# Optimization experiments

Hardware: AMD Instinct MI355X
Metric: run time of the kernel (lower is better)

Reference implementation:

```python
import jax, jax.numpy as jnp
import numpy as np
import math

B, NX, NY = 2, 2048, 2048
CX, CY = 1024, 1024
KEY_CH, VAL_CH, HEADS = 1024, 1024, 16


def setup_inputs() -> dict:
    key = jax.random.key(0)
    ks = jax.random.split(key, 10)
    s = lambda fan_in: 1.0 / math.sqrt(fan_in)
    inp = {
        "x": jax.random.normal(ks[0], (B, NX, CX), dtype=jnp.float32),
        "y": jax.random.normal(ks[1], (B, NY, CY), dtype=jnp.float32),
        "Wq": jax.random.uniform(ks[2], (CX, KEY_CH), jnp.float32, -s(CX), s(CX)),
        "bq": jax.random.uniform(ks[3], (KEY_CH,), jnp.float32, -s(CX), s(CX)),
        "Wk": jax.random.uniform(ks[4], (CY, KEY_CH), jnp.float32, -s(CY), s(CY)),
        "bk": jax.random.uniform(ks[5], (KEY_CH,), jnp.float32, -s(CY), s(CY)),
        "Wv": jax.random.uniform(ks[6], (CY, VAL_CH), jnp.float32, -s(CY), s(CY)),
        "bv": jax.random.uniform(ks[7], (VAL_CH,), jnp.float32, -s(CY), s(CY)),
        "Wo": jax.random.uniform(ks[8], (VAL_CH, CX), jnp.float32, -s(VAL_CH), s(VAL_CH)),
        "bo": jax.random.uniform(ks[9], (CX,), jnp.float32, -s(VAL_CH), s(VAL_CH)),
    }
    return inp


def reference(x, y, Wq, bq, Wk, bk, Wv, bv, Wo, bo):
    Bx, Nx, _ = x.shape
    By, Ny, _ = y.shape
    dk = KEY_CH // HEADS
    dv = VAL_CH // HEADS
    # projections
    q = (x @ Wq + bq).reshape(Bx, Nx, HEADS, dk)  # contiguous head slices == reshape
    k = (y @ Wk + bk).reshape(By, Ny, HEADS, dk)
    v = (y @ Wv + bv).reshape(By, Ny, HEADS, dv)
    # NOTE: original scales by 1/sqrt(Ny) (sequence length), not 1/sqrt(dk)
    scores = jnp.einsum("bnhd,bmhd->bhnm", q, k) / jnp.sqrt(jnp.float32(Ny))
    attn = jax.nn.softmax(scores, axis=-1)
    out = jnp.einsum("bhnm,bmhd->bnhd", attn, v).reshape(Bx, Nx, VAL_CH)
    out = jax.nn.relu(out @ Wo + bo)
    # dropout(p=0.2) is identity in eval mode
    return out
```

## Files before the change

kernel.cpp:

```cpp
#include <hip/hip_runtime.h>
#include <hip/hip_bf16.h>

typedef __bf16 bf16;
typedef __attribute__((ext_vector_type(8))) __bf16 bf16x8;
typedef __attribute__((ext_vector_type(4))) __bf16 bf16x4;
typedef __attribute__((ext_vector_type(4))) float f32x4;
typedef __attribute__((ext_vector_type(16))) float f32x16;
typedef __attribute__((ext_vector_type(4))) unsigned int u32x4;

__device__ __forceinline__ void gload_lds16(const void* g, void* l) {
  __builtin_amdgcn_global_load_lds((const __attribute__((address_space(1))) void*)g,
                                   (__attribute__((address_space(3))) void*)l, 16, 0, 0);
}

__device__ __forceinline__ float exp2_fast(float x) {
  float r;
  asm("v_exp_f32 %0, %1" : "=v"(r) : "v"(x));
  return r;
}

__device__ __forceinline__ unsigned cvtpk(float lo, float hi) {
  unsigned r;
  asm("v_cvt_pk_bf16_f32 %0, %1, %2" : "=v"(r) : "v"(lo), "v"(hi));
  return r;
}

__device__ __forceinline__ void plswap(unsigned& a, unsigned& b) {
  asm("v_permlane32_swap_b32 %0, %1" : "+v"(a), "+v"(b));
}

__global__ __launch_bounds__(256) void cvtw_kernel(
    const float* __restrict__ x, const float* __restrict__ y,
    bf16* __restrict__ xb, bf16* __restrict__ yb,
    const float* __restrict__ W0, const float* __restrict__ W1,
    const float* __restrict__ W2, const float* __restrict__ W3,
    bf16* __restrict__ T0, bf16* __restrict__ T1,
    bf16* __restrict__ T2, bf16* __restrict__ T3) {
  __shared__ float t[32][33];
  const int bid = blockIdx.x, tid = threadIdx.x;
  if (bid < 4096) {
    const int z = bid >> 10, rem = bid & 1023;
    const int bx = rem & 31, by = rem >> 5;
    const float* W; bf16* T;
    switch (z) {
      case 0: W = W0; T = T0; break;
      case 1: W = W1; T = T1; break;
      case 2: W = W2; T = T2; break;
      default: W = W3; T = T3; break;
    }
    const int tx = tid & 31, ty = tid >> 5;
    const int bn = bx * 32, bk = by * 32;
#pragma unroll
    for (int i = 0; i < 32; i += 8)
      t[ty + i][tx] = W[(size_t)(bk + ty + i) * 1024 + bn + tx];
    __syncthreads();
#pragma unroll
    for (int i = 0; i < 32; i += 8)
      T[(size_t)(bn + ty + i) * 1024 + bk + tx] = (bf16)t[tx][ty + i];
  } else {
    const int n4 = 1048576;
    int i = (bid - 4096) * 256 + tid;
    const float4* in = (const float4*)x; bf16x4* out = (bf16x4*)xb;
    if (i >= n4) { in = (const float4*)y; out = (bf16x4*)yb; i -= n4; }
    float4 v = in[i];
    bf16x4 o;
    o[0] = (bf16)v.x; o[1] = (bf16)v.y; o[2] = (bf16)v.z; o[3] = (bf16)v.w;
    out[i] = o;
  }
}

__global__ __launch_bounds__(512, 6) void gemm_qkv(
    const bf16* __restrict__ xb, const bf16* __restrict__ yb,
    const bf16* __restrict__ Wqt, const bf16* __restrict__ Wkt, const bf16* __restrict__ Wvt,
    const float* __restrict__ bq, const float* __restrict__ bk, const float* __restrict__ bv,
    bf16* __restrict__ Qb, bf16* __restrict__ Kb, bf16* __restrict__ Vtb) {
  constexpr int K = 1024;
  constexpr float QSCALE = (float)(1.4426950408889634 / 45.254833995939045);
  __shared__ bf16 As[2][128 * 32];
  __shared__ bf16 Bs[2][128 * 32];
  const int z = blockIdx.z;
  const bf16* A  = (z == 0) ? xb : yb;
  const bf16* Bt = (z == 0) ? Wqt : (z == 1) ? Wkt : Wvt;
  const float* bias = (z == 0) ? bq : (z == 1) ? bk : bv;

  const int tid = threadIdx.x;
  const int wave = tid >> 6, lane = tid & 63;
  const int g = lane >> 4, r15 = lane & 15;
  const int m0 = blockIdx.x * 128, n0 = blockIdx.y * 128;
  const int wr = wave >> 2, wc = wave & 3;

  f32x4 acc[4][2] = {};

  const int rowA = tid >> 2, chA = tid & 3;

  auto stage = [&](int buf, int k0) {
    gload_lds16(A  + (size_t)(m0 + rowA) * K + k0 + chA * 8, (char*)As[buf] + tid * 16);
    gload_lds16(Bt + (size_t)(n0 + rowA) * K + k0 + chA * 8, (char*)Bs[buf] + tid * 16);
  };

  stage(0, 0);
  __syncthreads();
  int cur = 0;
  for (int t = 0; t < K / 32; ++t) {
    if (t + 1 < K / 32) stage(cur ^ 1, (t + 1) * 32);
    bf16x8 af[4], bfr[2];
#pragma unroll
    for (int mi = 0; mi < 4; ++mi)
      af[mi] = *(const bf16x8*)((const char*)As[cur] + ((wr * 64 + mi * 16 + r15) * 64 + g * 16));
#pragma unroll
    for (int nj = 0; nj < 2; ++nj)
      bfr[nj] = *(const bf16x8*)((const char*)Bs[cur] + ((wc * 32 + nj * 16 + r15) * 64 + g * 16));
#pragma unroll
    for (int mi = 0; mi < 4; ++mi)
#pragma unroll
      for (int nj = 0; nj < 2; ++nj)
        acc[mi][nj] = __builtin_amdgcn_mfma_f32_16x16x32_bf16(af[mi], bfr[nj], acc[mi][nj], 0, 0, 0);
    __syncthreads();
    cur ^= 1;
  }

  const float scl = (z == 0) ? QSCALE : 1.0f;
#pragma unroll
  for (int mi = 0; mi < 4; ++mi) {
#pragma unroll
    for (int nj = 0; nj < 2; ++nj) {
      int row = m0 + wr * 64 + mi * 16 + g * 4;
      int col = n0 + wc * 32 + nj * 16 + r15;
      float bv_ = bias[col];
      if (z < 2) {
        bf16* C = (z == 0) ? Qb : Kb;
#pragma unroll
        for (int r = 0; r < 4; ++r)
          C[(size_t)(row + r) * 1024 + col] = (bf16)((acc[mi][nj][r] + bv_) * scl);
      } else {
        int b = row >> 11, n = row & 2047;
        bf16x4 pkv;
#pragma unroll
        for (int r = 0; r < 4; ++r)
          pkv[r] = (bf16)(acc[mi][nj][r] + bv_);
        *(bf16x4*)(Vtb + ((size_t)b * 1024 + col) * 2048 + n) = pkv;
      }
    }
  }
}

__global__ __launch_bounds__(512, 4) void gemm_out(
    const bf16* __restrict__ A, const bf16* __restrict__ Bt,
    const float* __restrict__ bias, float* __restrict__ C) {
  constexpr int K = 1024;
  __shared__ bf16 As[2][128 * 32];
  __shared__ bf16 Bs[2][64 * 32];
  const int tid = threadIdx.x;
  const int wave = tid >> 6, lane = tid & 63;
  const int g = lane >> 4, r15 = lane & 15;
  const int m0 = blockIdx.x * 128, n0 = blockIdx.y * 64;
  const int wr = wave >> 1, wc = wave & 1;

  f32x4 acc[2][2] = {};

  const int rowA = tid >> 2, chA = tid & 3;

  auto stage = [&](int buf, int k0) {
    gload_lds16(A + (size_t)(m0 + rowA) * K + k0 + chA * 8, (char*)As[buf] + tid * 16);
    if (tid < 256)
      gload_lds16(Bt + (size_t)(n0 + rowA) * K + k0 + chA * 8, (char*)Bs[buf] + tid * 16);
  };

  stage(0, 0);
  __syncthreads();
  int cur = 0;
  for (int t = 0; t < K / 32; ++t) {
    if (t + 1 < K / 32) stage(cur ^ 1, (t + 1) * 32);
    bf16x8 af[2], bfr[2];
#pragma unroll
    for (int mi = 0; mi < 2; ++mi)
      af[mi] = *(const bf16x8*)((const char*)As[cur] + ((wr * 32 + mi * 16 + r15) * 64 + g * 16));
#pragma unroll
    for (int nj = 0; nj < 2; ++nj)
      bfr[nj] = *(const bf16x8*)((const char*)Bs[cur] + ((wc * 32 + nj * 16 + r15) * 64 + g * 16));
#pragma unroll
    for (int mi = 0; mi < 2; ++mi)
#pragma unroll
      for (int nj = 0; nj < 2; ++nj)
        acc[mi][nj] = __builtin_amdgcn_mfma_f32_16x16x32_bf16(af[mi], bfr[nj], acc[mi][nj], 0, 0, 0);
    __syncthreads();
    cur ^= 1;
  }

#pragma unroll
  for (int mi = 0; mi < 2; ++mi)
#pragma unroll
    for (int nj = 0; nj < 2; ++nj) {
      int row = m0 + wr * 32 + mi * 16 + g * 4;
      int col = n0 + wc * 32 + nj * 16 + r15;
      float bv_ = bias[col];
#pragma unroll
      for (int r = 0; r < 4; ++r)
        C[(size_t)(row + r) * 1024 + col] = fmaxf(acc[mi][nj][r] + bv_, 0.0f);
    }
}

__global__ __launch_bounds__(128, 2) void attn_kernel(
    const bf16* __restrict__ Q, const bf16* __restrict__ Kin,
    const bf16* __restrict__ Vt, bf16* __restrict__ Oa) {
  __shared__ bf16 Ks[2][64 * 64];
  __shared__ bf16 Vs[2][64 * 64];
  __shared__ float lsh[2][2][32];
  const int tid = threadIdx.x;
  const int w = tid >> 6, lane = tid & 63;
  const int q5 = lane & 31, h = lane >> 5;

  int i = blockIdx.y * 32 + blockIdx.x;
  int xcd = i & 7, slot = i >> 3;
  int bh = xcd * 4 + (slot >> 5), qt = slot & 31;
  int b = bh >> 4, hd = bh & 15;

  const bf16* Qg = Q + ((size_t)b * 2048 + qt * 64) * 1024 + hd * 64;
  const bf16* Kg = Kin + (size_t)b * 2048 * 1024 + hd * 64;
  const bf16* Vg = Vt + ((size_t)b * 1024 + hd * 64) * 2048;

  bf16x8 qf[2][4];
#pragma unroll
  for (int qb = 0; qb < 2; ++qb)
#pragma unroll
    for (int ks = 0; ks < 4; ++ks)
      qf[qb][ks] = *(const bf16x8*)(Qg + (size_t)(qb * 32 + q5) * 1024 + ks * 16 + h * 8);

  f32x16 o[2][2] = {};
  float ls[2] = {};

  auto stage = [&](int buf, int kv0) {
#pragma unroll
    for (int ii = 0; ii < 4; ++ii) {
      int c = tid + ii * 128;
      int row = c >> 3;
      int sl = (c & 7) ^ (row & 7) ^ ((row >> 3) & 1);
      gload_lds16(Kg + (size_t)(kv0 + row) * 1024 + sl * 8, (char*)Ks[buf] + c * 16);
      gload_lds16(Vg + (size_t)row * 2048 + kv0 + sl * 8, (char*)Vs[buf] + c * 16);
    }
  };

  stage(0, 0);
  __syncthreads();
  int cur = 0;

  const int krow = w * 32 + q5;
  const int kswz = (krow & 7) ^ ((krow >> 3) & 1);

  unsigned uA[2][8], uB[2][8];
  bf16x8 vA[4], vB[4];

  auto phase = [&](int t, unsigned (&uin)[2][8], unsigned (&uout)[2][8],
                   bf16x8 (&vin)[4], bf16x8 (&vout)[4], bool doStage, bool doPV) {
    if (doStage) stage(cur ^ 1, (t + 1) * 64);

    f32x16 s[2] = {};
    __builtin_amdgcn_s_setprio(1);
#pragma unroll
    for (int ks = 0; ks < 4; ++ks) {
      bf16x8 kf = *(const bf16x8*)((const char*)Ks[cur] + krow * 128 + (((2 * ks + h) ^ kswz) << 4));
      s[0] = __builtin_amdgcn_mfma_f32_32x32x16_bf16(kf, qf[0][ks], s[0], 0, 0, 0);
      s[1] = __builtin_amdgcn_mfma_f32_32x32x16_bf16(kf, qf[1][ks], s[1], 0, 0, 0);
    }

#pragma unroll
    for (int j = 0; j < 2; ++j) {
      const int db = w ^ j;
      const int vrow0 = db * 32 + q5;
      const int vswz = (vrow0 & 7) ^ ((vrow0 >> 3) & 1);
#pragma unroll
      for (int kap = 0; kap < 2; ++kap)
        vout[2 * j + kap] = *(const bf16x8*)((const char*)Vs[cur] + vrow0 * 128 +
                                             (((4 * w + 2 * kap + h) ^ vswz) << 4));
    }

    if (doPV) {
#pragma unroll
      for (int j = 0; j < 2; ++j)
#pragma unroll
        for (int kap = 0; kap < 2; ++kap)
#pragma unroll
          for (int qb = 0; qb < 2; ++qb) {
            u32x4 uw;
            uw[0] = uin[qb][4 * kap + 0]; uw[1] = uin[qb][4 * kap + 1];
            uw[2] = uin[qb][4 * kap + 2]; uw[3] = uin[qb][4 * kap + 3];
            bf16x8 pa = __builtin_bit_cast(bf16x8, uw);
            o[qb][j] = __builtin_amdgcn_mfma_f32_32x32x16_bf16(pa, vin[2 * j + kap], o[qb][j], 0, 0, 0);
          }
    }
    __builtin_amdgcn_s_setprio(0);

#pragma unroll
    for (int qb = 0; qb < 2; ++qb) {
      float e[16];
#pragma unroll
      for (int jj = 0; jj < 16; ++jj) e[jj] = exp2_fast(s[qb][jj]);
      ls[qb] += ((((e[0] + e[1]) + (e[2] + e[3])) + ((e[4] + e[5]) + (e[6] + e[7]))) +
                 (((e[8] + e[9]) + (e[10] + e[11])) + ((e[12] + e[13]) + (e[14] + e[15]))));
#pragma unroll
      for (int p = 0; p < 8; ++p) uout[qb][p] = cvtpk(e[2 * p], e[2 * p + 1]);
      plswap(uout[qb][0], uout[qb][2]); plswap(uout[qb][1], uout[qb][3]);
      plswap(uout[qb][4], uout[qb][6]); plswap(uout[qb][5], uout[qb][7]);
    }

    __syncthreads();
    cur ^= 1;
  };

  phase(0, uB, uA, vB, vA, true, false);
  for (int t = 1; t < 31; t += 2) {
    phase(t, uA, uB, vA, vB, true, true);
    phase(t + 1, uB, uA, vB, vA, true, true);
  }
  phase(31, uA, uB, vA, vB, false, true);
#pragma unroll
  for (int j = 0; j < 2; ++j)
#pragma unroll
    for (int kap = 0; kap < 2; ++kap)
#pragma unroll
      for (int qb = 0; qb < 2; ++qb) {
        u32x4 uw;
        uw[0] = uB[qb][4 * kap + 0]; uw[1] = uB[qb][4 * kap + 1];
        uw[2] = uB[qb][4 * kap + 2]; uw[3] = uB[qb][4 * kap + 3];
        bf16x8 pa = __builtin_bit_cast(bf16x8, uw);
        o[qb][j] = __builtin_amdgcn_mfma_f32_32x32x16_bf16(pa, vB[2 * j + kap], o[qb][j], 0, 0, 0);
      }

  ls[0] += __shfl_xor(ls[0], 32);
  ls[1] += __shfl_xor(ls[1], 32);
  if (h == 0) { lsh[w][0][q5] = ls[0]; lsh[w][1][q5] = ls[1]; }

  float* osh = (float*)Ks;
#pragma unroll
  for (int qb = 0; qb < 2; ++qb)
    *(f32x16*)(osh + ((w * 2 + qb) * 64 + lane) * 16) = o[qb][1];
  __syncthreads();

#pragma unroll
  for (int qb = 0; qb < 2; ++qb) {
    float lt = ls[qb] + lsh[1 - w][qb][q5];
    float iv = __builtin_amdgcn_rcpf(lt);
    f32x16 p = *(const f32x16*)(osh + (((1 - w) * 2 + qb) * 64 + lane) * 16);
#pragma unroll
    for (int g4 = 0; g4 < 4; ++g4)
#pragma unroll
      for (int r = 0; r < 4; ++r) {
        int qr = g4 * 8 + 4 * h + r;
        float il = __shfl(iv, qr);
        size_t row = (size_t)b * 2048 + qt * 64 + qb * 32 + qr;
        Oa[row * 1024 + hd * 64 + w * 32 + q5] = (bf16)((o[qb][0][g4 * 4 + r] + p[g4 * 4 + r]) * il);
      }
  }
}

extern "C" void kernel_launch(void* const* d_in, const int* in_sizes, int n_in,
                              void* d_out, int out_size, void* d_ws, size_t ws_size,
                              hipStream_t stream) {
  (void)in_sizes; (void)n_in; (void)out_size; (void)ws_size;
  const float* x  = (const float*)d_in[0];
  const float* y  = (const float*)d_in[1];
  const float* Wq = (const float*)d_in[2];
  const float* bq = (const float*)d_in[3];
  const float* Wk = (const float*)d_in[4];
  const float* bk = (const float*)d_in[5];
  const float* Wv = (const float*)d_in[6];
  const float* bv = (const float*)d_in[7];
  const float* Wo = (const float*)d_in[8];
  const float* bo = (const float*)d_in[9];

  char* ws = (char*)d_ws;
  bf16* xb  = (bf16*)(ws + 0);
  bf16* yb  = (bf16*)(ws + 8388608);
  bf16* Qb  = (bf16*)(ws + 16777216);
  bf16* Kb  = (bf16*)(ws + 25165824);
  bf16* Vtb = (bf16*)(ws + 33554432);
  bf16* Oab = (bf16*)(ws + 41943040);
  bf16* Wqt = (bf16*)(ws + 50331648);
  bf16* Wkt = (bf16*)(ws + 52428800);
  bf16* Wvt = (bf16*)(ws + 54525952);
  bf16* Wot = (bf16*)(ws + 56623104);

  cvtw_kernel<<<12288, 256, 0, stream>>>(x, y, xb, yb, Wq, Wk, Wv, Wo, Wqt, Wkt, Wvt, Wot);
  gemm_qkv<<<dim3(32, 8, 3), 512, 0, stream>>>(xb, yb, Wqt, Wkt, Wvt, bq, bk, bv, Qb, Kb, Vtb);
  attn_kernel<<<dim3(32, 32), dim3(128), 0, stream>>>(Qb, Kb, Vtb, Oab);
  gemm_out<<<dim3(32, 16), 512, 0, stream>>>(Oab, Wot, bo, (float*)d_out);
}
```

Before: 117.9 us.

## Halve attention query tile, load V directly from global, raise occupancy

The attention kernel now handles 32 query rows per block instead of 64, which doubles the grid and halves the per-thread registers for scores, outputs and row sums, so launch bounds ask for 4 blocks per SIMD. V is no longer staged through LDS; each wave reads its V fragments straight from global memory, which frees shared memory for higher occupancy. The inline-asm exp and permlane swap are replaced by compiler builtins. In exchange, K and V are re-read twice as often across the grid, and the direct global V loads sit in the PV path without prefetch, which may add latency.

```diff
diff --git a/kernel.cpp b/kernel.cpp
--- a/kernel.cpp
+++ b/kernel.cpp
@@ -7,26 +7,22 @@
 typedef __attribute__((ext_vector_type(4))) float f32x4;
 typedef __attribute__((ext_vector_type(16))) float f32x16;
 typedef __attribute__((ext_vector_type(4))) unsigned int u32x4;
+typedef __attribute__((ext_vector_type(2))) unsigned int u32x2;
 
 __device__ __forceinline__ void gload_lds16(const void* g, void* l) {
   __builtin_amdgcn_global_load_lds((const __attribute__((address_space(1))) void*)g,
                                    (__attribute__((address_space(3))) void*)l, 16, 0, 0);
 }
 
-__device__ __forceinline__ float exp2_fast(float x) {
-  float r;
-  asm("v_exp_f32 %0, %1" : "=v"(r) : "v"(x));
-  return r;
-}
-
+__device__ __forceinline__ float exp2_b(float x) { return __builtin_amdgcn_exp2f(x); }
+__device__ __forceinline__ void plswap_b(unsigned& a, unsigned& b) {
+  u32x2 r = __builtin_amdgcn_permlane32_swap(a, b, false, false);
+  a = r[0]; b = r[1];
+}
 __device__ __forceinline__ unsigned cvtpk(float lo, float hi) {
   unsigned r;
   asm("v_cvt_pk_bf16_f32 %0, %1, %2" : "=v"(r) : "v"(lo), "v"(hi));
   return r;
-}
-
-__device__ __forceinline__ void plswap(unsigned& a, unsigned& b) {
-  asm("v_permlane32_swap_b32 %0, %1" : "+v"(a), "+v"(b));
 }
 
 __global__ __launch_bounds__(256) void cvtw_kernel(
@@ -200,34 +196,31 @@
     }
 }
 
-__global__ __launch_bounds__(128, 2) void attn_kernel(
+__global__ __launch_bounds__(128, 4) void attn_kernel(
     const bf16* __restrict__ Q, const bf16* __restrict__ Kin,
     const bf16* __restrict__ Vt, bf16* __restrict__ Oa) {
   __shared__ bf16 Ks[2][64 * 64];
-  __shared__ bf16 Vs[2][64 * 64];
-  __shared__ float lsh[2][2][32];
+  __shared__ float lsh[2][32];
   const int tid = threadIdx.x;
   const int w = tid >> 6, lane = tid & 63;
   const int q5 = lane & 31, h = lane >> 5;
 
-  int i = blockIdx.y * 32 + blockIdx.x;
+  int i = blockIdx.y * 64 + blockIdx.x;
   int xcd = i & 7, slot = i >> 3;
-  int bh = xcd * 4 + (slot >> 5), qt = slot & 31;
+  int bh = xcd * 4 + (slot >> 6), qt = slot & 63;
   int b = bh >> 4, hd = bh & 15;
 
-  const bf16* Qg = Q + ((size_t)b * 2048 + qt * 64) * 1024 + hd * 64;
+  const bf16* Qg = Q + ((size_t)b * 2048 + qt * 32) * 1024 + hd * 64;
   const bf16* Kg = Kin + (size_t)b * 2048 * 1024 + hd * 64;
   const bf16* Vg = Vt + ((size_t)b * 1024 + hd * 64) * 2048;
 
-  bf16x8 qf[2][4];
-#pragma unroll
-  for (int qb = 0; qb < 2; ++qb)
-#pragma unroll
-    for (int ks = 0; ks < 4; ++ks)
-      qf[qb][ks] = *(const bf16x8*)(Qg + (size_t)(qb * 32 + q5) * 1024 + ks * 16 + h * 8);
-
-  f32x16 o[2][2] = {};
-  float ls[2] = {};
+  bf16x8 qf[4];
+#pragma unroll
+  for (int ks = 0; ks < 4; ++ks)
+    qf[ks] = *(const bf16x8*)(Qg + (size_t)q5 * 1024 + ks * 16 + h * 8);
+
+  f32x16 o[2] = {};
+  float ls = 0.0f;
 
   auto stage = [&](int buf, int kv0) {
 #pragma unroll
@@ -236,7 +229,6 @@
       int row = c >> 3;
       int sl = (c & 7) ^ (row & 7) ^ ((row >> 3) & 1);
       gload_lds16(Kg + (size_t)(kv0 + row) * 1024 + sl * 8, (char*)Ks[buf] + c * 16);
-      gload_lds16(Vg + (size_t)row * 2048 + kv0 + sl * 8, (char*)Vs[buf] + c * 16);
     }
   };
 
@@ -247,61 +239,53 @@
   const int krow = w * 32 + q5;
   const int kswz = (krow & 7) ^ ((krow >> 3) & 1);
 
-  unsigned uA[2][8], uB[2][8];
+  unsigned uA[8], uB[8];
   bf16x8 vA[4], vB[4];
 
-  auto phase = [&](int t, unsigned (&uin)[2][8], unsigned (&uout)[2][8],
+  auto phase = [&](int t, unsigned (&uin)[8], unsigned (&uout)[8],
                    bf16x8 (&vin)[4], bf16x8 (&vout)[4], bool doStage, bool doPV) {
     if (doStage) stage(cur ^ 1, (t + 1) * 64);
 
-    f32x16 s[2] = {};
+    f32x16 s = {};
     __builtin_amdgcn_s_setprio(1);
 #pragma unroll
     for (int ks = 0; ks < 4; ++ks) {
       bf16x8 kf = *(const bf16x8*)((const char*)Ks[cur] + krow * 128 + (((2 * ks + h) ^ kswz) << 4));
-      s[0] = __builtin_amdgcn_mfma_f32_32x32x16_bf16(kf, qf[0][ks], s[0], 0, 0, 0);
-      s[1] = __builtin_amdgcn_mfma_f32_32x32x16_bf16(kf, qf[1][ks], s[1], 0, 0, 0);
+      s = __builtin_amdgcn_mfma_f32_32x32x16_bf16(kf, qf[ks], s, 0, 0, 0);
     }
 
 #pragma unroll
     for (int j = 0; j < 2; ++j) {
       const int db = w ^ j;
-      const int vrow0 = db * 32 + q5;
-      const int vswz = (vrow0 & 7) ^ ((vrow0 >> 3) & 1);
 #pragma unroll
       for (int kap = 0; kap < 2; ++kap)
-        vout[2 * j + kap] = *(const bf16x8*)((const char*)Vs[cur] + vrow0 * 128 +
-                                             (((4 * w + 2 * kap + h) ^ vswz) << 4));
+        vout[2 * j + kap] = *(const bf16x8*)(Vg + (size_t)(db * 32 + q5) * 2048 +
+                                            t * 64 + (4 * w + 2 * kap + h) * 8);
     }
 
     if (doPV) {
 #pragma unroll
       for (int j = 0; j < 2; ++j)
 #pragma unroll
-        for (int kap = 0; kap < 2; ++kap)
-#pragma unroll
-          for (int qb = 0; qb < 2; ++qb) {
-            u32x4 uw;
-            uw[0] = uin[qb][4 * kap + 0]; uw[1] = uin[qb][4 * kap + 1];
-            uw[2] = uin[qb][4 * kap + 2]; uw[3] = uin[qb][4 * kap + 3];
-            bf16x8 pa = __builtin_bit_cast(bf16x8, uw);
-            o[qb][j] = __builtin_amdgcn_mfma_f32_32x32x16_bf16(pa, vin[2 * j + kap], o[qb][j], 0, 0, 0);
-          }
+        for (int kap = 0; kap < 2; ++kap) {
+          u32x4 uw;
+          uw[0] = uin[4 * kap + 0]; uw[1] = uin[4 * kap + 1];
+          uw[2] = uin[4 * kap + 2]; uw[3] = uin[4 * kap + 3];
+          bf16x8 pa = __builtin_bit_cast(bf16x8, uw);
+          o[j] = __builtin_amdgcn_mfma_f32_32x32x16_bf16(pa, vin[2 * j + kap], o[j], 0, 0, 0);
+        }
     }
     __builtin_amdgcn_s_setprio(0);
 
-#pragma unroll
-    for (int qb = 0; qb < 2; ++qb) {
-      float e[16];
-#pragma unroll
-      for (int jj = 0; jj < 16; ++jj) e[jj] = exp2_fast(s[qb][jj]);
-      ls[qb] += ((((e[0] + e[1]) + (e[2] + e[3])) + ((e[4] + e[5]) + (e[6] + e[7]))) +
-                 (((e[8] + e[9]) + (e[10] + e[11])) + ((e[12] + e[13]) + (e[14] + e[15]))));
-#pragma unroll
-      for (int p = 0; p < 8; ++p) uout[qb][p] = cvtpk(e[2 * p], e[2 * p + 1]);
-      plswap(uout[qb][0], uout[qb][2]); plswap(uout[qb][1], uout[qb][3]);
-      plswap(uout[qb][4], uout[qb][6]); plswap(uout[qb][5], uout[qb][7]);
-    }
+    float e[16];
+#pragma unroll
+    for (int jj = 0; jj < 16; ++jj) e[jj] = exp2_b(s[jj]);
+    ls += ((((e[0] + e[1]) + (e[2] + e[3])) + ((e[4] + e[5]) + (e[6] + e[7]))) +
+           (((e[8] + e[9]) + (e[10] + e[11])) + ((e[12] + e[13]) + (e[14] + e[15]))));
+#pragma unroll
+    for (int p = 0; p < 8; ++p) uout[p] = cvtpk(e[2 * p], e[2 * p + 1]);
+    plswap_b(uout[0], uout[2]); plswap_b(uout[1], uout[3]);
+    plswap_b(uout[4], uout[6]); plswap_b(uout[5], uout[7]);
 
     __syncthreads();
     cur ^= 1;
@@ -316,41 +300,34 @@
 #pragma unroll
   for (int j = 0; j < 2; ++j)
 #pragma unroll
-    for (int kap = 0; kap < 2; ++kap)
-#pragma unroll
-      for (int qb = 0; qb < 2; ++qb) {
-        u32x4 uw;
-        uw[0] = uB[qb][4 * kap + 0]; uw[1] = uB[qb][4 * kap + 1];
-        uw[2] = uB[qb][4 * kap + 2]; uw[3] = uB[qb][4 * kap + 3];
-        bf16x8 pa = __builtin_bit_cast(bf16x8, uw);
-        o[qb][j] = __builtin_amdgcn_mfma_f32_32x32x16_bf16(pa, vB[2 * j + kap], o[qb][j], 0, 0, 0);
-      }
-
-  ls[0] += __shfl_xor(ls[0], 32);
-  ls[1] += __shfl_xor(ls[1], 32);
-  if (h == 0) { lsh[w][0][q5] = ls[0]; lsh[w][1][q5] = ls[1]; }
+    for (int kap = 0; kap < 2; ++kap) {
+      u32x4 uw;
+      uw[0] = uB[4 * kap + 0]; uw[1] = uB[4 * kap + 1];
+      uw[2] = uB[4 * kap + 2]; uw[3] = uB[4 * kap + 3];
+      bf16x8 pa = __builtin_bit_cast(bf16x8, uw);
+      o[j] = __builtin_amdgcn_mfma_f32_32x32x16_bf16(pa, vB[2 * j + kap], o[j], 0, 0, 0);
+    }
+
+  ls += __shfl_xor(ls, 32);
+  if (h == 0) lsh[w][q5] = ls;
 
   float* osh = (float*)Ks;
-#pragma unroll
-  for (int qb = 0; qb < 2; ++qb)
-    *(f32x16*)(osh + ((w * 2 + qb) * 64 + lane) * 16) = o[qb][1];
+  *(f32x16*)(osh + ((size_t)(w * 64 + lane)) * 16) = o[1];
   __syncthreads();
 
-#pragma unroll
-  for (int qb = 0; qb < 2; ++qb) {
-    float lt = ls[qb] + lsh[1 - w][qb][q5];
-    float iv = __builtin_amdgcn_rcpf(lt);
-    f32x16 p = *(const f32x16*)(osh + (((1 - w) * 2 + qb) * 64 + lane) * 16);
-#pragma unroll
-    for (int g4 = 0; g4 < 4; ++g4)
-#pragma unroll
-      for (int r = 0; r < 4; ++r) {
-        int qr = g4 * 8 + 4 * h + r;
-        float il = __shfl(iv, qr);
-        size_t row = (size_t)b * 2048 + qt * 64 + qb * 32 + qr;
-        Oa[row * 1024 + hd * 64 + w * 32 + q5] = (bf16)((o[qb][0][g4 * 4 + r] + p[g4 * 4 + r]) * il);
-      }
-  }
+  const int pw = 1 - w;
+  float lt = ls + lsh[pw][q5];
+  float iv = __builtin_amdgcn_rcpf(lt);
+  f32x16 p = *(const f32x16*)(osh + ((size_t)(pw * 64 + lane)) * 16);
+#pragma unroll
+  for (int g4 = 0; g4 < 4; ++g4)
+#pragma unroll
+    for (int r = 0; r < 4; ++r) {
+      int qr = g4 * 8 + 4 * h + r;
+      float il = __shfl(iv, qr);
+      size_t row = (size_t)b * 2048 + qt * 32 + qr;
+      Oa[row * 1024 + hd * 64 + w * 32 + q5] = (bf16)((o[0][g4 * 4 + r] + p[g4 * 4 + r]) * il);
+    }
 }
 
 extern "C" void kernel_launch(void* const* d_in, const int* in_sizes, int n_in,
@@ -382,6 +359,6 @@
 
   cvtw_kernel<<<12288, 256, 0, stream>>>(x, y, xb, yb, Wq, Wk, Wv, Wo, Wqt, Wkt, Wvt, Wot);
   gemm_qkv<<<dim3(32, 8, 3), 512, 0, stream>>>(xb, yb, Wqt, Wkt, Wvt, bq, bk, bv, Qb, Kb, Vtb);
-  attn_kernel<<<dim3(32, 32), dim3(128), 0, stream>>>(Qb, Kb, Vtb, Oab);
+  attn_kernel<<<dim3(64, 32), dim3(128), 0, stream>>>(Qb, Kb, Vtb, Oab);
   gemm_out<<<dim3(32, 16), 512, 0, stream>>>(Oab, Wot, bo, (float*)d_out);
 }
```

Result: slower. 148.5 us (+26.0%).
